# Performance work log

Hardware: AMD Instinct MI355X
Metric: run time of the kernel (lower is better)

The kernel has to match this reference:

```python
import jax, jax.numpy as jnp
import numpy as np

HEADS = 8
WS = 8  # window size


def conv1x1(x, w, b):
    # x: [B,C,H,W], w: [Cout,Cin], b: [Cout]
    return jnp.einsum('bchw,oc->bohw', x, w) + b[None, :, None, None]


def to_windows(x, heads, ws):
    # x: [B,C,H,W] -> [B*nH*nW, heads, ws*ws, C//heads]
    B, C, H, W = x.shape
    d = C // heads
    x = x.reshape(B, heads, d, H // ws, ws, W // ws, ws)
    x = x.transpose(0, 3, 5, 1, 4, 6, 2)  # B, nH, nW, heads, ws, ws, d
    return x.reshape(B * (H // ws) * (W // ws), heads, ws * ws, d)


def from_windows(xw, B, C, H, W, heads, ws):
    d = C // heads
    x = xw.reshape(B, H // ws, W // ws, heads, ws, ws, d)
    x = x.transpose(0, 3, 6, 1, 4, 2, 5)  # B, heads, d, nH, ws, nW, ws
    return x.reshape(B, C, H, W)


def setup_inputs() -> dict:
    key = jax.random.key(0)
    ks = jax.random.split(key, 10)
    B, C, H, W = 4, 256, 256, 256
    s = 0.02
    return {
        'q_feat': jax.random.normal(ks[0], (B, C, H, W), jnp.float32),
        'kv_feat': jax.random.normal(ks[1], (B, C, H, W), jnp.float32),
        'wq': jax.random.normal(ks[2], (C, C), jnp.float32) * s,
        'bq': jnp.zeros((C,), jnp.float32),
        'wk': jax.random.normal(ks[3], (C, C), jnp.float32) * s,
        'bk': jnp.zeros((C,), jnp.float32),
        'wv': jax.random.normal(ks[4], (C, C), jnp.float32) * s,
        'bv': jnp.zeros((C,), jnp.float32),
        'wp': jax.random.normal(ks[5], (C, C), jnp.float32) * s,
        'bp': jnp.zeros((C,), jnp.float32),
    }


def reference(q_feat, kv_feat, wq, bq, wk, bk, wv, bv, wp, bp):
    B, C, H, W = q_feat.shape
    heads, ws = HEADS, WS
    scale = (C // heads) ** (-0.5)

    q = to_windows(conv1x1(q_feat, wq, bq), heads, ws)   # [Nw, h, ws*ws, d]
    k = to_windows(conv1x1(kv_feat, wk, bk), heads, ws)
    v = to_windows(conv1x1(kv_feat, wv, bv), heads, ws)

    attn = jnp.einsum('whqd,whkd->whqk', q, k) * scale
    attn = jax.nn.softmax(attn, axis=-1)
    out_w = jnp.einsum('whqk,whkd->whqd', attn, v)

    out = from_windows(out_w, B, C, H, W, heads, ws)
    return conv1x1(out, wp, bp)
```

## Files before the change

kernel.cpp:

```cpp
#include <hip/hip_runtime.h>
#include <cstdint>
#include <cstddef>


typedef __attribute__((ext_vector_type(8))) short bfx8;
typedef __attribute__((ext_vector_type(4))) float f32x4;

#define HW 65536
#define NC 256
#define QKV_STRIDE 16777216UL

__device__ __forceinline__ unsigned short f2bf(float f) {
  union { float f; unsigned u; } v; v.f = f;
  unsigned r = v.u + 0x7FFFu + ((v.u >> 16) & 1u);
  return (unsigned short)(r >> 16);
}

__global__ __launch_bounds__(256) void prep_weights(
    const float* __restrict__ wq, const float* __restrict__ wk,
    const float* __restrict__ wv, const float* __restrict__ wp,
    unsigned short* __restrict__ dst) {
  int i = blockIdx.x * 256 + threadIdx.x;
  dst[i]          = f2bf(wq[i]);
  dst[i + 65536]  = f2bf(wk[i]);
  dst[i + 131072] = f2bf(wv[i]);
  dst[i + 196608] = f2bf(wp[i]);
}

__device__ __forceinline__ void gemm_pass(
    const unsigned short* __restrict__ wmat, const unsigned char* __restrict__ smem,
    int wid, int g, int qh, f32x4 (&acc)[4][4]) {
#pragma unroll
  for (int i = 0; i < 4; ++i)
#pragma unroll
    for (int j = 0; j < 4; ++j) acc[i][j] = (f32x4){0.f, 0.f, 0.f, 0.f};

  bfx8 afr[4];
#pragma unroll
  for (int mt = 0; mt < 4; ++mt)
    afr[mt] = *(const bfx8*)(wmat + (wid * 64 + mt * 16 + qh) * 256 + g * 8);

  for (int ks = 0; ks < 8; ++ks) {
    bfx8 naf[4];
    if (ks < 7) {
#pragma unroll
      for (int mt = 0; mt < 4; ++mt)
        naf[mt] = *(const bfx8*)(wmat + (wid * 64 + mt * 16 + qh) * 256 + (ks + 1) * 32 + g * 8);
    }
#pragma unroll
    for (int nt = 0; nt < 4; ++nt) {
      unsigned byte = ((unsigned)((nt * 16 + qh) * 512 + ks * 64 + g * 16)) ^
                      (((unsigned)(qh & 7)) << 4);
      bfx8 bfr = *(const bfx8*)(smem + byte);
#pragma unroll
      for (int mt = 0; mt < 4; ++mt)
        acc[mt][nt] = __builtin_amdgcn_mfma_f32_16x16x32_bf16(afr[mt], bfr, acc[mt][nt], 0, 0, 0);
    }
    if (ks < 7) {
#pragma unroll
      for (int mt = 0; mt < 4; ++mt) afr[mt] = naf[mt];
    }
  }
}

__device__ __forceinline__ void store_qk(
    const f32x4 (&acc)[4][4], const float* __restrict__ bias,
    unsigned short* __restrict__ outw, int n0, int wid, int g, int qh) {
  const int h_img = n0 >> 8, w0b = n0 & 255;
#pragma unroll
  for (int mt = 0; mt < 4; ++mt) {
    int o = wid * 64 + mt * 16 + g * 4;
    f32x4 bb = *(const f32x4*)&bias[o];
    int head = o >> 5, dbase = o & 31;
#pragma unroll
    for (int nt = 0; nt < 4; ++nt) {
      int n = nt * 16 + qh;
      int w_img = w0b + n;
      int win = ((h_img >> 3) << 5) + (w_img >> 3);
      int pos = ((h_img & 7) << 3) + (w_img & 7);
      f32x4 a = acc[mt][nt];
      uint2 pv;
      pv.x = (unsigned)f2bf(a.x + bb.x) | ((unsigned)f2bf(a.y + bb.y) << 16);
      pv.y = (unsigned)f2bf(a.z + bb.z) | ((unsigned)f2bf(a.w + bb.w) << 16);
      *(uint2*)&outw[((size_t)(win * 8 + head) * 64 + pos) * 32 + dbase] = pv;
    }
  }
}

__global__ __launch_bounds__(256) void qkv_gemm(
    const float* __restrict__ xq, const float* __restrict__ xkv,
    const unsigned short* __restrict__ wbf,
    const float* __restrict__ bq, const float* __restrict__ bk,
    const float* __restrict__ bv,
    unsigned short* __restrict__ q_w, unsigned short* __restrict__ k_w,
    unsigned short* __restrict__ v_w, int batch0, int batched) {
  __shared__ __align__(16) unsigned char smem[36864];

  const int tid = threadIdx.x;
  const int lane = tid & 63;
  const int wid = tid >> 6;
  const int g = lane >> 4;
  const int qh = lane & 15;
  const int mode = blockIdx.x & 1;
  const int n0 = (int)(blockIdx.x >> 1) * 64;
  const int batch = batch0 + blockIdx.z;
  const size_t qofs = batched ? (size_t)blockIdx.z * QKV_STRIDE : 0;
  const float* x = (mode ? xkv : xq) + (size_t)batch * NC * HW;

  {
    const int sn = tid & 63;
    const int oc = tid >> 6;
#pragma unroll
    for (int it = 0; it < 8; ++it) {
      int c8 = (it * 4 + oc) * 8;
      const float* xp = x + (size_t)c8 * HW + n0 + sn;
      float v0 = xp[0],      v1 = xp[HW],     v2 = xp[2 * HW], v3 = xp[3 * HW];
      float v4 = xp[4 * HW], v5 = xp[5 * HW], v6 = xp[6 * HW], v7 = xp[7 * HW];
      uint4 u;
      u.x = (unsigned)f2bf(v0) | ((unsigned)f2bf(v1) << 16);
      u.y = (unsigned)f2bf(v2) | ((unsigned)f2bf(v3) << 16);
      u.z = (unsigned)f2bf(v4) | ((unsigned)f2bf(v5) << 16);
      u.w = (unsigned)f2bf(v6) | ((unsigned)f2bf(v7) << 16);
      unsigned byte = ((unsigned)(sn * 512 + c8 * 2)) ^ (((unsigned)(sn & 7)) << 4);
      *(uint4*)(smem + byte) = u;
    }
  }
  __syncthreads();

  f32x4 acc[4][4];
  if (mode == 0) {
    gemm_pass(wbf, smem, wid, g, qh, acc);
    store_qk(acc, bq, q_w + qofs, n0, wid, g, qh);
  } else {
    gemm_pass(wbf + 65536, smem, wid, g, qh, acc);
    store_qk(acc, bk, k_w + qofs, n0, wid, g, qh);
    gemm_pass(wbf + 131072, smem, wid, g, qh, acc);
    __syncthreads();
    unsigned short* Vt = (unsigned short*)smem;
#pragma unroll
    for (int mt = 0; mt < 4; ++mt) {
      int o = wid * 64 + mt * 16 + g * 4;
      f32x4 bb = *(const f32x4*)&bv[o];
#pragma unroll
      for (int nt = 0; nt < 4; ++nt) {
        int n = nt * 16 + qh;
        f32x4 a = acc[mt][nt];
        Vt[(o + 0) * 72 + n] = f2bf(a.x + bb.x);
        Vt[(o + 1) * 72 + n] = f2bf(a.y + bb.y);
        Vt[(o + 2) * 72 + n] = f2bf(a.z + bb.z);
        Vt[(o + 3) * 72 + n] = f2bf(a.w + bb.w);
      }
    }
    __syncthreads();
    const int h_img = n0 >> 8, w0b = n0 & 255;
    unsigned short* vw = v_w + qofs;
#pragma unroll
    for (int it = 0; it < 8; ++it) {
      int id = it * 256 + tid;
      int o = id >> 3, oct = id & 7;
      uint4 val = *(const uint4*)&Vt[o * 72 + oct * 8];
      int head = o >> 5, dd = o & 31;
      int win = ((h_img >> 3) << 5) + (w0b >> 3) + oct;
      *(uint4*)&vw[((size_t)(win * 8 + head) * 32 + dd) * 64 + ((h_img & 7) << 3)] = val;
    }
  }
}

__global__ __launch_bounds__(256) void attn_conv(
    const unsigned short* __restrict__ q_w, const unsigned short* __restrict__ k_w,
    const unsigned short* __restrict__ v_w, const unsigned short* __restrict__ wpbf,
    const float* __restrict__ bp, float* __restrict__ out, int batch0, int batched) {
  __shared__ unsigned short P_lds[4][2048];
  __shared__ unsigned short y_t[16384];

  const int tid = threadIdx.x;
  const int lane = tid & 63;
  const int wid = tid >> 6;
  const int g = lane >> 4;
  const int qh = lane & 15;
  const int bid = blockIdx.x;
  const int winl = ((bid & 7) << 7) | (bid >> 3);
  const int batch = batch0 + blockIdx.z;
  const size_t qofs = batched ? (size_t)blockIdx.z * QKV_STRIDE : 0;
  const float scale = 0.17677669529663687f;

  char* pbase = (char*)&P_lds[wid][0];

#pragma unroll
  for (int hi = 0; hi < 2; ++hi) {
    const int head = wid + hi * 4;
    const unsigned short* qb = q_w + qofs + (size_t)(winl * 8 + head) * 2048;
    const unsigned short* kb = k_w + qofs + (size_t)(winl * 8 + head) * 2048;
    const unsigned short* vb = v_w + qofs + (size_t)(winl * 8 + head) * 2048;

    bfx8 kf[4], qf[4];
#pragma unroll
    for (int t = 0; t < 4; ++t) {
      kf[t] = *(const bfx8*)(kb + (t * 16 + qh) * 32 + g * 8);
      qf[t] = *(const bfx8*)(qb + (t * 16 + qh) * 32 + g * 8);
    }
    f32x4 zero = {0.f, 0.f, 0.f, 0.f};
    f32x4 st[4][4];
#pragma unroll
    for (int kt = 0; kt < 4; ++kt)
#pragma unroll
      for (int qt = 0; qt < 4; ++qt)
        st[kt][qt] = __builtin_amdgcn_mfma_f32_16x16x32_bf16(kf[kt], qf[qt], zero, 0, 0, 0);

    float rv[4];
#pragma unroll
    for (int qt = 0; qt < 4; ++qt) {
      float m = -1e30f;
#pragma unroll
      for (int kt = 0; kt < 4; ++kt) {
        f32x4 v = st[kt][qt];
        m = fmaxf(m, fmaxf(fmaxf(v.x, v.y), fmaxf(v.z, v.w)));
      }
      m = fmaxf(m, __shfl_xor(m, 16, 64));
      m = fmaxf(m, __shfl_xor(m, 32, 64));
      float ssum = 0.f;
#pragma unroll
      for (int kt = 0; kt < 4; ++kt) {
        f32x4 v = st[kt][qt], e;
        e.x = __expf((v.x - m) * scale);
        e.y = __expf((v.y - m) * scale);
        e.z = __expf((v.z - m) * scale);
        e.w = __expf((v.w - m) * scale);
        ssum += e.x + e.y + e.z + e.w;
        st[kt][qt] = e;
      }
      ssum += __shfl_xor(ssum, 16, 64);
      ssum += __shfl_xor(ssum, 32, 64);
      rv[qt] = 1.f / ssum;
    }

    f32x4 ot[2][4];
#pragma unroll
    for (int dt = 0; dt < 2; ++dt)
#pragma unroll
      for (int qt = 0; qt < 4; ++qt) ot[dt][qt] = zero;

#pragma unroll
    for (int s = 0; s < 2; ++s) {
#pragma unroll
      for (int qt = 0; qt < 4; ++qt) {
        int q = qt * 16 + qh;
        unsigned sw = ((unsigned)(q & 3)) << 4;
        float r = rv[qt];
#pragma unroll
        for (int k2 = 0; k2 < 2; ++k2) {
          f32x4 e = st[s * 2 + k2][qt];
          uint2 pv;
          pv.x = (unsigned)f2bf(e.x * r) | ((unsigned)f2bf(e.y * r) << 16);
          pv.y = (unsigned)f2bf(e.z * r) | ((unsigned)f2bf(e.w * r) << 16);
          unsigned byte = ((unsigned)q * 64 + (unsigned)(k2 * 32 + g * 8)) ^ sw;
          *(uint2*)(pbase + byte) = pv;
        }
      }
      bfx8 pf[4];
#pragma unroll
      for (int qt = 0; qt < 4; ++qt) {
        int q = qt * 16 + qh;
        unsigned byte = ((unsigned)q * 64 + (unsigned)(g * 16)) ^ (((unsigned)(q & 3)) << 4);
        pf[qt] = *(const bfx8*)(pbase + byte);
      }
#pragma unroll
      for (int dt = 0; dt < 2; ++dt) {
        bfx8 vf = *(const bfx8*)(vb + (dt * 16 + qh) * 64 + s * 32 + g * 8);
#pragma unroll
        for (int qt = 0; qt < 4; ++qt)
          ot[dt][qt] = __builtin_amdgcn_mfma_f32_16x16x32_bf16(vf, pf[qt], ot[dt][qt], 0, 0, 0);
      }
    }

#pragma unroll
    for (int dt = 0; dt < 2; ++dt) {
      int cb = head * 32 + dt * 16 + g * 4;
#pragma unroll
      for (int qt = 0; qt < 4; ++qt) {
        int pos = qt * 16 + qh;
        f32x4 a = ot[dt][qt];
        uint2 pv;
        pv.x = (unsigned)f2bf(a.x) | ((unsigned)f2bf(a.y) << 16);
        pv.y = (unsigned)f2bf(a.z) | ((unsigned)f2bf(a.w) << 16);
        unsigned byte = ((unsigned)pos * 512 + (unsigned)cb * 2) ^ (((unsigned)(pos & 7)) << 4);
        *(uint2*)((char*)y_t + byte) = pv;
      }
    }
  }
  __syncthreads();

  f32x4 acc[4][4];
#pragma unroll
  for (int i = 0; i < 4; ++i)
#pragma unroll
    for (int j = 0; j < 4; ++j) acc[i][j] = (f32x4){0.f, 0.f, 0.f, 0.f};

  for (int ks = 0; ks < 8; ++ks) {
    bfx8 af[4];
#pragma unroll
    for (int mt = 0; mt < 4; ++mt)
      af[mt] = *(const bfx8*)(wpbf + (wid * 64 + mt * 16 + qh) * 256 + ks * 32 + g * 8);
#pragma unroll
    for (int nt = 0; nt < 4; ++nt) {
      int pos = nt * 16 + qh;
      unsigned byte = ((unsigned)pos * 512 + (unsigned)(ks * 64 + g * 16)) ^ (((unsigned)(pos & 7)) << 4);
      bfx8 bfr = *(const bfx8*)((char*)y_t + byte);
#pragma unroll
      for (int mt = 0; mt < 4; ++mt)
        acc[mt][nt] = __builtin_amdgcn_mfma_f32_16x16x32_bf16(af[mt], bfr, acc[mt][nt], 0, 0, 0);
    }
  }

  const int wrow = winl >> 5, wcol = winl & 31;
  float* ob_ = out + (size_t)batch * NC * HW;
#pragma unroll
  for (int mt = 0; mt < 4; ++mt) {
    int o0 = wid * 64 + mt * 16 + g * 4;
    float b0 = bp[o0], b1 = bp[o0 + 1], b2 = bp[o0 + 2], b3 = bp[o0 + 3];
#pragma unroll
    for (int nt = 0; nt < 4; ++nt) {
      int pos = nt * 16 + qh;
      int h_img = wrow * 8 + (pos >> 3);
      int w_img = wcol * 8 + (pos & 7);
      float* pp = ob_ + (size_t)o0 * HW + h_img * 256 + w_img;
      pp[0]      = acc[mt][nt].x + b0;
      pp[HW]     = acc[mt][nt].y + b1;
      pp[2 * HW] = acc[mt][nt].z + b2;
      pp[3 * HW] = acc[mt][nt].w + b3;
    }
  }
}

extern "C" void kernel_launch(void* const* d_in, const int* in_sizes, int n_in,
                              void* d_out, int out_size, void* d_ws, size_t ws_size,
                              hipStream_t stream) {
  const float* q_feat = (const float*)d_in[0];
  const float* kv_feat = (const float*)d_in[1];
  const float* wq = (const float*)d_in[2];
  const float* bq = (const float*)d_in[3];
  const float* wk = (const float*)d_in[4];
  const float* bk = (const float*)d_in[5];
  const float* wv = (const float*)d_in[6];
  const float* bv = (const float*)d_in[7];
  const float* wp = (const float*)d_in[8];
  const float* bp = (const float*)d_in[9];
  float* out = (float*)d_out;

  unsigned short* wbf = (unsigned short*)d_ws;
  const size_t need_batched = 524288ul + 12ul * QKV_STRIDE * 2ul;

  hipLaunchKernelGGL(prep_weights, dim3(256), dim3(256), 0, stream, wq, wk, wv, wp, wbf);

  if (ws_size >= need_batched) {
    unsigned short* q_w = wbf + 262144;
    unsigned short* k_w = q_w + 4 * QKV_STRIDE;
    unsigned short* v_w = k_w + 4 * QKV_STRIDE;
    hipLaunchKernelGGL(qkv_gemm, dim3(2048, 1, 4), dim3(256), 0, stream,
                       q_feat, kv_feat, wbf, bq, bk, bv, q_w, k_w, v_w, 0, 1);
    hipLaunchKernelGGL(attn_conv, dim3(1024, 1, 4), dim3(256), 0, stream,
                       q_w, k_w, v_w, wbf + 196608, bp, out, 0, 1);
  } else {
    unsigned short* q_w = wbf + 262144;
    unsigned short* k_w = q_w + QKV_STRIDE;
    unsigned short* v_w = k_w + QKV_STRIDE;
    for (int b = 0; b < 4; ++b) {
      hipLaunchKernelGGL(qkv_gemm, dim3(2048, 1, 1), dim3(256), 0, stream,
                         q_feat, kv_feat, wbf, bq, bk, bv, q_w, k_w, v_w, b, 0);
      hipLaunchKernelGGL(attn_conv, dim3(1024, 1, 1), dim3(256), 0, stream,
                         q_w, k_w, v_w, wbf + 196608, bp, out, b, 0);
    }
  }
}
```

Baseline: 632.2 us.

## Pre-tile weights into MFMA fragment order and vectorize QKV input staging

The weight conversion kernel now writes bf16 weights in a per-lane MFMA fragment order, so each wave's A-operand loads become contiguous 16-byte-per-lane reads instead of strided row accesses. The QKV projection kernel now loads inputs as float4 along the spatial dimension, with each thread covering 16 channels. It uses a new LDS XOR swizzle (n ^ n>>2) to keep the transposed stores conflict-free. This aims to cut global load transactions and LDS bank conflicts, at the cost of more registers per thread for the staged inputs.

Result: slower. 645.2 us (+2.1%).

```diff
diff --git a/kernel.cpp b/kernel.cpp
--- a/kernel.cpp
+++ b/kernel.cpp
@@ -14,6 +14,10 @@
   union { float f; unsigned u; } v; v.f = f;
   unsigned r = v.u + 0x7FFFu + ((v.u >> 16) & 1u);
   return (unsigned short)(r >> 16);
+}
+
+__device__ __forceinline__ unsigned xswz(unsigned n) {
+  return ((n ^ (n >> 2)) & 7u) << 4;
 }
 
 __global__ __launch_bounds__(256) void prep_weights(
@@ -21,15 +25,17 @@
     const float* __restrict__ wv, const float* __restrict__ wp,
     unsigned short* __restrict__ dst) {
   int i = blockIdx.x * 256 + threadIdx.x;
-  dst[i]          = f2bf(wq[i]);
-  dst[i + 65536]  = f2bf(wk[i]);
-  dst[i + 131072] = f2bf(wv[i]);
-  dst[i + 196608] = f2bf(wp[i]);
+  int e = i & 7, lane = (i >> 3) & 63, ks = (i >> 9) & 7, ot = i >> 12;
+  int src = (ot * 16 + (lane & 15)) * 256 + ks * 32 + (lane >> 4) * 8 + e;
+  dst[i]          = f2bf(wq[src]);
+  dst[i + 65536]  = f2bf(wk[src]);
+  dst[i + 131072] = f2bf(wv[src]);
+  dst[i + 196608] = f2bf(wp[src]);
 }
 
 __device__ __forceinline__ void gemm_pass(
-    const unsigned short* __restrict__ wmat, const unsigned char* __restrict__ smem,
-    int wid, int g, int qh, f32x4 (&acc)[4][4]) {
+    const unsigned short* __restrict__ wT, const unsigned char* __restrict__ smem,
+    int wid, int lane, int g, int qh, f32x4 (&acc)[4][4]) {
 #pragma unroll
   for (int i = 0; i < 4; ++i)
 #pragma unroll
@@ -38,19 +44,19 @@
   bfx8 afr[4];
 #pragma unroll
   for (int mt = 0; mt < 4; ++mt)
-    afr[mt] = *(const bfx8*)(wmat + (wid * 64 + mt * 16 + qh) * 256 + g * 8);
+    afr[mt] = *(const bfx8*)(wT + (((wid * 4 + mt) * 8 + 0) * 64 + lane) * 8);
 
   for (int ks = 0; ks < 8; ++ks) {
     bfx8 naf[4];
     if (ks < 7) {
 #pragma unroll
       for (int mt = 0; mt < 4; ++mt)
-        naf[mt] = *(const bfx8*)(wmat + (wid * 64 + mt * 16 + qh) * 256 + (ks + 1) * 32 + g * 8);
+        naf[mt] = *(const bfx8*)(wT + (((wid * 4 + mt) * 8 + ks + 1) * 64 + lane) * 8);
     }
 #pragma unroll
     for (int nt = 0; nt < 4; ++nt) {
-      unsigned byte = ((unsigned)((nt * 16 + qh) * 512 + ks * 64 + g * 16)) ^
-                      (((unsigned)(qh & 7)) << 4);
+      unsigned n = (unsigned)(nt * 16 + qh);
+      unsigned byte = (n * 512 + (unsigned)(ks * 64 + g * 16)) ^ xswz(n);
       bfx8 bfr = *(const bfx8*)(smem + byte);
 #pragma unroll
       for (int mt = 0; mt < 4; ++mt)
@@ -108,33 +114,42 @@
   const float* x = (mode ? xkv : xq) + (size_t)batch * NC * HW;
 
   {
-    const int sn = tid & 63;
-    const int oc = tid >> 6;
-#pragma unroll
-    for (int it = 0; it < 8; ++it) {
-      int c8 = (it * 4 + oc) * 8;
-      const float* xp = x + (size_t)c8 * HW + n0 + sn;
-      float v0 = xp[0],      v1 = xp[HW],     v2 = xp[2 * HW], v3 = xp[3 * HW];
-      float v4 = xp[4 * HW], v5 = xp[5 * HW], v6 = xp[6 * HW], v7 = xp[7 * HW];
+    const int n4 = lane & 15;
+    const int c8a = wid * 4 + (lane >> 4);
+    const float* xp0 = x + (size_t)(c8a * 8) * HW + n0 + n4 * 4;
+    const float* xp1 = xp0 + (size_t)128 * HW;
+    f32x4 r0[8], r1[8];
+#pragma unroll
+    for (int i = 0; i < 8; ++i) r0[i] = *(const f32x4*)(xp0 + (size_t)i * HW);
+#pragma unroll
+    for (int i = 0; i < 8; ++i) r1[i] = *(const f32x4*)(xp1 + (size_t)i * HW);
+#pragma unroll
+    for (int e = 0; e < 4; ++e) {
+      unsigned n = (unsigned)(n4 * 4 + e);
       uint4 u;
-      u.x = (unsigned)f2bf(v0) | ((unsigned)f2bf(v1) << 16);
-      u.y = (unsigned)f2bf(v2) | ((unsigned)f2bf(v3) << 16);
-      u.z = (unsigned)f2bf(v4) | ((unsigned)f2bf(v5) << 16);
-      u.w = (unsigned)f2bf(v6) | ((unsigned)f2bf(v7) << 16);
-      unsigned byte = ((unsigned)(sn * 512 + c8 * 2)) ^ (((unsigned)(sn & 7)) << 4);
-      *(uint4*)(smem + byte) = u;
+      u.x = (unsigned)f2bf(r0[0][e]) | ((unsigned)f2bf(r0[1][e]) << 16);
+      u.y = (unsigned)f2bf(r0[2][e]) | ((unsigned)f2bf(r0[3][e]) << 16);
+      u.z = (unsigned)f2bf(r0[4][e]) | ((unsigned)f2bf(r0[5][e]) << 16);
+      u.w = (unsigned)f2bf(r0[6][e]) | ((unsigned)f2bf(r0[7][e]) << 16);
+      *(uint4*)(smem + ((n * 512 + (unsigned)c8a * 16) ^ xswz(n))) = u;
+      uint4 v;
+      v.x = (unsigned)f2bf(r1[0][e]) | ((unsigned)f2bf(r1[1][e]) << 16);
+      v.y = (unsigned)f2bf(r1[2][e]) | ((unsigned)f2bf(r1[3][e]) << 16);
+      v.z = (unsigned)f2bf(r1[4][e]) | ((unsigned)f2bf(r1[5][e]) << 16);
+      v.w = (unsigned)f2bf(r1[6][e]) | ((unsigned)f2bf(r1[7][e]) << 16);
+      *(uint4*)(smem + ((n * 512 + (unsigned)(c8a + 16) * 16) ^ xswz(n))) = v;
     }
   }
   __syncthreads();
 
   f32x4 acc[4][4];
   if (mode == 0) {
-    gemm_pass(wbf, smem, wid, g, qh, acc);
+    gemm_pass(wbf, smem, wid, lane, g, qh, acc);
     store_qk(acc, bq, q_w + qofs, n0, wid, g, qh);
   } else {
-    gemm_pass(wbf + 65536, smem, wid, g, qh, acc);
+    gemm_pass(wbf + 65536, smem, wid, lane, g, qh, acc);
     store_qk(acc, bk, k_w + qofs, n0, wid, g, qh);
-    gemm_pass(wbf + 131072, smem, wid, g, qh, acc);
+    gemm_pass(wbf + 131072, smem, wid, lane, g, qh, acc);
     __syncthreads();
     unsigned short* Vt = (unsigned short*)smem;
 #pragma unroll
@@ -168,7 +183,7 @@
 
 __global__ __launch_bounds__(256) void attn_conv(
     const unsigned short* __restrict__ q_w, const unsigned short* __restrict__ k_w,
-    const unsigned short* __restrict__ v_w, const unsigned short* __restrict__ wpbf,
+    const unsigned short* __restrict__ v_w, const unsigned short* __restrict__ wpT,
     const float* __restrict__ bp, float* __restrict__ out, int batch0, int batched) {
   __shared__ unsigned short P_lds[4][2048];
   __shared__ unsigned short y_t[16384];
@@ -300,7 +315,7 @@
     bfx8 af[4];
 #pragma unroll
     for (int mt = 0; mt < 4; ++mt)
-      af[mt] = *(const bfx8*)(wpbf + (wid * 64 + mt * 16 + qh) * 256 + ks * 32 + g * 8);
+      af[mt] = *(const bfx8*)(wpT + (((wid * 4 + mt) * 8 + ks) * 64 + lane) * 8);
 #pragma unroll
     for (int nt = 0; nt < 4; ++nt) {
       int pos = nt * 16 + qh;
```

## Stage Q/K stores through LDS, pre-swizzle Wp, process four windows per attention block

Applied to the files above, without the earlier changes.

The Q/K epilogue now writes its tiles into a separate LDS buffer and then emits 16-byte coalesced global stores per window/head row, replacing scattered 8-byte stores. The projection weight is pre-permuted into the MFMA fragment order so each lane loads its A fragment contiguously. The attention kernel now loops over four adjacent windows per block with a quarter of the blocks, which gives wider contiguous runs on output rows and reuses weight loads in cache. The cost is more LDS per block in qkv_gemm, which may lower occupancy, and fewer, longer attention blocks with extra barriers.

New measurement: 743.9 us. +17.7%, slower.

```diff
diff --git a/kernel.cpp b/kernel.cpp
--- a/kernel.cpp
+++ b/kernel.cpp
@@ -24,7 +24,29 @@
   dst[i]          = f2bf(wq[i]);
   dst[i + 65536]  = f2bf(wk[i]);
   dst[i + 131072] = f2bf(wv[i]);
-  dst[i + 196608] = f2bf(wp[i]);
+  int e = i & 7, lane = (i >> 3) & 63, ks = (i >> 9) & 7, ot = i >> 12;
+  int src = (ot * 16 + (lane & 15)) * 256 + ks * 32 + (lane >> 4) * 8 + e;
+  dst[i + 196608] = f2bf(wp[src]);
+}
+
+__device__ __forceinline__ void stage_x(
+    const float* __restrict__ x, int n0, int tid, unsigned char* __restrict__ smem) {
+  const int sn = tid & 63;
+  const int oc = tid >> 6;
+#pragma unroll
+  for (int it = 0; it < 8; ++it) {
+    int c8 = (it * 4 + oc) * 8;
+    const float* xp = x + (size_t)c8 * HW + n0 + sn;
+    float v0 = xp[0],      v1 = xp[HW],     v2 = xp[2 * HW], v3 = xp[3 * HW];
+    float v4 = xp[4 * HW], v5 = xp[5 * HW], v6 = xp[6 * HW], v7 = xp[7 * HW];
+    uint4 u;
+    u.x = (unsigned)f2bf(v0) | ((unsigned)f2bf(v1) << 16);
+    u.y = (unsigned)f2bf(v2) | ((unsigned)f2bf(v3) << 16);
+    u.z = (unsigned)f2bf(v4) | ((unsigned)f2bf(v5) << 16);
+    u.w = (unsigned)f2bf(v6) | ((unsigned)f2bf(v7) << 16);
+    unsigned byte = ((unsigned)(sn * 512 + c8 * 2)) ^ (((unsigned)(sn & 7)) << 4);
+    *(uint4*)(smem + byte) = u;
+  }
 }
 
 __device__ __forceinline__ void gemm_pass(
@@ -63,27 +85,41 @@
   }
 }
 
-__device__ __forceinline__ void store_qk(
+__device__ __forceinline__ void epi_qk_store(
     const f32x4 (&acc)[4][4], const float* __restrict__ bias,
-    unsigned short* __restrict__ outw, int n0, int wid, int g, int qh) {
-  const int h_img = n0 >> 8, w0b = n0 & 255;
+    unsigned short* __restrict__ outw, int n0, int wid, int g, int qh, int tid,
+    unsigned char* __restrict__ epi) {
+  const int h7 = (n0 >> 8) & 7;
+  const int w0b = n0 & 255;
 #pragma unroll
   for (int mt = 0; mt < 4; ++mt) {
     int o = wid * 64 + mt * 16 + g * 4;
     f32x4 bb = *(const f32x4*)&bias[o];
     int head = o >> 5, dbase = o & 31;
+    unsigned hs = (unsigned)(head & 7) << 4;
 #pragma unroll
     for (int nt = 0; nt < 4; ++nt) {
       int n = nt * 16 + qh;
-      int w_img = w0b + n;
-      int win = ((h_img >> 3) << 5) + (w_img >> 3);
-      int pos = ((h_img & 7) << 3) + (w_img & 7);
+      unsigned byte = ((unsigned)((n >> 3) * 4096 + head * 512 + (n & 7) * 64 + dbase * 2)) ^ hs;
       f32x4 a = acc[mt][nt];
       uint2 pv;
       pv.x = (unsigned)f2bf(a.x + bb.x) | ((unsigned)f2bf(a.y + bb.y) << 16);
       pv.y = (unsigned)f2bf(a.z + bb.z) | ((unsigned)f2bf(a.w + bb.w) << 16);
-      *(uint2*)&outw[((size_t)(win * 8 + head) * 64 + pos) * 32 + dbase] = pv;
-    }
+      *(uint2*)(epi + byte) = pv;
+    }
+  }
+  __syncthreads();
+  const int r = tid >> 2, lane4 = tid & 3;
+  const int winIdx = r >> 3, head = r & 7;
+  const unsigned hs = (unsigned)(head & 7) << 4;
+  const int win = ((n0 >> 8) >> 3) * 32 + (w0b >> 3) + winIdx;
+  unsigned short* gdst = outw + (size_t)(win * 8 + head) * 2048 + h7 * 256;
+  const unsigned char* src = epi + winIdx * 4096 + head * 512;
+#pragma unroll
+  for (int it = 0; it < 8; ++it) {
+    unsigned off = (unsigned)(it * 64 + lane4 * 16);
+    uint4 v = *(const uint4*)(src + (off ^ hs));
+    *(uint4*)&gdst[it * 32 + lane4 * 8] = v;
   }
 }
 
@@ -94,7 +130,8 @@
     const float* __restrict__ bv,
     unsigned short* __restrict__ q_w, unsigned short* __restrict__ k_w,
     unsigned short* __restrict__ v_w, int batch0, int batched) {
-  __shared__ __align__(16) unsigned char smem[36864];
+  __shared__ __align__(16) unsigned char smem[32768];
+  __shared__ __align__(16) unsigned char epi[36864];
 
   const int tid = threadIdx.x;
   const int lane = tid & 63;
@@ -107,36 +144,19 @@
   const size_t qofs = batched ? (size_t)blockIdx.z * QKV_STRIDE : 0;
   const float* x = (mode ? xkv : xq) + (size_t)batch * NC * HW;
 
-  {
-    const int sn = tid & 63;
-    const int oc = tid >> 6;
-#pragma unroll
-    for (int it = 0; it < 8; ++it) {
-      int c8 = (it * 4 + oc) * 8;
-      const float* xp = x + (size_t)c8 * HW + n0 + sn;
-      float v0 = xp[0],      v1 = xp[HW],     v2 = xp[2 * HW], v3 = xp[3 * HW];
-      float v4 = xp[4 * HW], v5 = xp[5 * HW], v6 = xp[6 * HW], v7 = xp[7 * HW];
-      uint4 u;
-      u.x = (unsigned)f2bf(v0) | ((unsigned)f2bf(v1) << 16);
-      u.y = (unsigned)f2bf(v2) | ((unsigned)f2bf(v3) << 16);
-      u.z = (unsigned)f2bf(v4) | ((unsigned)f2bf(v5) << 16);
-      u.w = (unsigned)f2bf(v6) | ((unsigned)f2bf(v7) << 16);
-      unsigned byte = ((unsigned)(sn * 512 + c8 * 2)) ^ (((unsigned)(sn & 7)) << 4);
-      *(uint4*)(smem + byte) = u;
-    }
-  }
+  stage_x(x, n0, tid, smem);
   __syncthreads();
 
   f32x4 acc[4][4];
   if (mode == 0) {
     gemm_pass(wbf, smem, wid, g, qh, acc);
-    store_qk(acc, bq, q_w + qofs, n0, wid, g, qh);
+    epi_qk_store(acc, bq, q_w + qofs, n0, wid, g, qh, tid, epi);
   } else {
     gemm_pass(wbf + 65536, smem, wid, g, qh, acc);
-    store_qk(acc, bk, k_w + qofs, n0, wid, g, qh);
+    epi_qk_store(acc, bk, k_w + qofs, n0, wid, g, qh, tid, epi);
     gemm_pass(wbf + 131072, smem, wid, g, qh, acc);
     __syncthreads();
-    unsigned short* Vt = (unsigned short*)smem;
+    unsigned short* Vt = (unsigned short*)epi;
 #pragma unroll
     for (int mt = 0; mt < 4; ++mt) {
       int o = wid * 64 + mt * 16 + g * 4;
@@ -168,7 +188,7 @@
 
 __global__ __launch_bounds__(256) void attn_conv(
     const unsigned short* __restrict__ q_w, const unsigned short* __restrict__ k_w,
-    const unsigned short* __restrict__ v_w, const unsigned short* __restrict__ wpbf,
+    const unsigned short* __restrict__ v_w, const unsigned short* __restrict__ wpT,
     const float* __restrict__ bp, float* __restrict__ out, int batch0, int batched) {
   __shared__ unsigned short P_lds[4][2048];
   __shared__ unsigned short y_t[16384];
@@ -179,155 +199,161 @@
   const int g = lane >> 4;
   const int qh = lane & 15;
   const int bid = blockIdx.x;
-  const int winl = ((bid & 7) << 7) | (bid >> 3);
+  const int wrow = bid >> 3;
+  const int wcol0 = (bid & 7) * 4;
   const int batch = batch0 + blockIdx.z;
   const size_t qofs = batched ? (size_t)blockIdx.z * QKV_STRIDE : 0;
   const float scale = 0.17677669529663687f;
 
   char* pbase = (char*)&P_lds[wid][0];
-
-#pragma unroll
-  for (int hi = 0; hi < 2; ++hi) {
-    const int head = wid + hi * 4;
-    const unsigned short* qb = q_w + qofs + (size_t)(winl * 8 + head) * 2048;
-    const unsigned short* kb = k_w + qofs + (size_t)(winl * 8 + head) * 2048;
-    const unsigned short* vb = v_w + qofs + (size_t)(winl * 8 + head) * 2048;
-
-    bfx8 kf[4], qf[4];
-#pragma unroll
-    for (int t = 0; t < 4; ++t) {
-      kf[t] = *(const bfx8*)(kb + (t * 16 + qh) * 32 + g * 8);
-      qf[t] = *(const bfx8*)(qb + (t * 16 + qh) * 32 + g * 8);
-    }
-    f32x4 zero = {0.f, 0.f, 0.f, 0.f};
-    f32x4 st[4][4];
-#pragma unroll
-    for (int kt = 0; kt < 4; ++kt)
-#pragma unroll
-      for (int qt = 0; qt < 4; ++qt)
-        st[kt][qt] = __builtin_amdgcn_mfma_f32_16x16x32_bf16(kf[kt], qf[qt], zero, 0, 0, 0);
-
-    float rv[4];
-#pragma unroll
-    for (int qt = 0; qt < 4; ++qt) {
-      float m = -1e30f;
-#pragma unroll
-      for (int kt = 0; kt < 4; ++kt) {
-        f32x4 v = st[kt][qt];
-        m = fmaxf(m, fmaxf(fmaxf(v.x, v.y), fmaxf(v.z, v.w)));
-      }
-      m = fmaxf(m, __shfl_xor(m, 16, 64));
-      m = fmaxf(m, __shfl_xor(m, 32, 64));
-      float ssum = 0.f;
-#pragma unroll
-      for (int kt = 0; kt < 4; ++kt) {
-        f32x4 v = st[kt][qt], e;
-        e.x = __expf((v.x - m) * scale);
-        e.y = __expf((v.y - m) * scale);
-        e.z = __expf((v.z - m) * scale);
-        e.w = __expf((v.w - m) * scale);
-        ssum += e.x + e.y + e.z + e.w;
-        st[kt][qt] = e;
-      }
-      ssum += __shfl_xor(ssum, 16, 64);
-      ssum += __shfl_xor(ssum, 32, 64);
-      rv[qt] = 1.f / ssum;
-    }
-
-    f32x4 ot[2][4];
-#pragma unroll
-    for (int dt = 0; dt < 2; ++dt)
-#pragma unroll
-      for (int qt = 0; qt < 4; ++qt) ot[dt][qt] = zero;
-
-#pragma unroll
-    for (int s = 0; s < 2; ++s) {
+  float* ob_ = out + (size_t)batch * NC * HW;
+
+  for (int wi = 0; wi < 4; ++wi) {
+    if (wi) __syncthreads();
+    const int winl = wrow * 32 + wcol0 + wi;
+
+#pragma unroll
+    for (int hi = 0; hi < 2; ++hi) {
+      const int head = wid + hi * 4;
+      const unsigned short* qb = q_w + qofs + (size_t)(winl * 8 + head) * 2048;
+      const unsigned short* kb = k_w + qofs + (size_t)(winl * 8 + head) * 2048;
+      const unsigned short* vb = v_w + qofs + (size_t)(winl * 8 + head) * 2048;
+
+      bfx8 kf[4], qf[4];
+#pragma unroll
+      for (int t = 0; t < 4; ++t) {
+        kf[t] = *(const bfx8*)(kb + (t * 16 + qh) * 32 + g * 8);
+        qf[t] = *(const bfx8*)(qb + (t * 16 + qh) * 32 + g * 8);
+      }
+      f32x4 zero = {0.f, 0.f, 0.f, 0.f};
+      f32x4 st[4][4];
+#pragma unroll
+      for (int kt = 0; kt < 4; ++kt)
+#pragma unroll
+        for (int qt = 0; qt < 4; ++qt)
+          st[kt][qt] = __builtin_amdgcn_mfma_f32_16x16x32_bf16(kf[kt], qf[qt], zero, 0, 0, 0);
+
+      float rv[4];
 #pragma unroll
       for (int qt = 0; qt < 4; ++qt) {
-        int q = qt * 16 + qh;
-        unsigned sw = ((unsigned)(q & 3)) << 4;
-        float r = rv[qt];
-#pragma unroll
-        for (int k2 = 0; k2 < 2; ++k2) {
-          f32x4 e = st[s * 2 + k2][qt];
+        float m = -1e30f;
+#pragma unroll
+        for (int kt = 0; kt < 4; ++kt) {
+          f32x4 v = st[kt][qt];
+          m = fmaxf(m, fmaxf(fmaxf(v.x, v.y), fmaxf(v.z, v.w)));
+        }
+        m = fmaxf(m, __shfl_xor(m, 16, 64));
+        m = fmaxf(m, __shfl_xor(m, 32, 64));
+        float ssum = 0.f;
+#pragma unroll
+        for (int kt = 0; kt < 4; ++kt) {
+          f32x4 v = st[kt][qt], e;
+          e.x = __expf((v.x - m) * scale);
+          e.y = __expf((v.y - m) * scale);
+          e.z = __expf((v.z - m) * scale);
+          e.w = __expf((v.w - m) * scale);
+          ssum += e.x + e.y + e.z + e.w;
+          st[kt][qt] = e;
+        }
+        ssum += __shfl_xor(ssum, 16, 64);
+        ssum += __shfl_xor(ssum, 32, 64);
+        rv[qt] = 1.f / ssum;
+      }
+
+      f32x4 ot[2][4];
+#pragma unroll
+      for (int dt = 0; dt < 2; ++dt)
+#pragma unroll
+        for (int qt = 0; qt < 4; ++qt) ot[dt][qt] = zero;
+
+#pragma unroll
+      for (int s = 0; s < 2; ++s) {
+#pragma unroll
+        for (int qt = 0; qt < 4; ++qt) {
+          int q = qt * 16 + qh;
+          unsigned sw = ((unsigned)(q & 3)) << 4;
+          float r = rv[qt];
+#pragma unroll
+          for (int k2 = 0; k2 < 2; ++k2) {
+            f32x4 e = st[s * 2 + k2][qt];
+            uint2 pv;
+            pv.x = (unsigned)f2bf(e.x * r) | ((unsigned)f2bf(e.y * r) << 16);
+            pv.y = (unsigned)f2bf(e.z * r) | ((unsigned)f2bf(e.w * r) << 16);
+            unsigned byte = ((unsigned)q * 64 + (unsigned)(k2 * 32 + g * 8)) ^ sw;
+            *(uint2*)(pbase + byte) = pv;
+          }
+        }
+        bfx8 pf[4];
+#pragma unroll
+        for (int qt = 0; qt < 4; ++qt) {
+          int q = qt * 16 + qh;
+          unsigned byte = ((unsigned)q * 64 + (unsigned)(g * 16)) ^ (((unsigned)(q & 3)) << 4);
+          pf[qt] = *(const bfx8*)(pbase + byte);
+        }
+#pragma unroll
+        for (int dt = 0; dt < 2; ++dt) {
+          bfx8 vf = *(const bfx8*)(vb + (dt * 16 + qh) * 64 + s * 32 + g * 8);
+#pragma unroll
+          for (int qt = 0; qt < 4; ++qt)
+            ot[dt][qt] = __builtin_amdgcn_mfma_f32_16x16x32_bf16(vf, pf[qt], ot[dt][qt], 0, 0, 0);
+        }
+      }
+
+#pragma unroll
+      for (int dt = 0; dt < 2; ++dt) {
+        int cb = head * 32 + dt * 16 + g * 4;
+#pragma unroll
+        for (int qt = 0; qt < 4; ++qt) {
+          int pos = qt * 16 + qh;
+          f32x4 a = ot[dt][qt];
           uint2 pv;
-          pv.x = (unsigned)f2bf(e.x * r) | ((unsigned)f2bf(e.y * r) << 16);
-          pv.y = (unsigned)f2bf(e.z * r) | ((unsigned)f2bf(e.w * r) << 16);
-          unsigned byte = ((unsigned)q * 64 + (unsigned)(k2 * 32 + g * 8)) ^ sw;
-          *(uint2*)(pbase + byte) = pv;
-        }
-      }
-      bfx8 pf[4];
-#pragma unroll
-      for (int qt = 0; qt < 4; ++qt) {
-        int q = qt * 16 + qh;
-        unsigned byte = ((unsigned)q * 64 + (unsigned)(g * 16)) ^ (((unsigned)(q & 3)) << 4);
-        pf[qt] = *(const bfx8*)(pbase + byte);
-      }
-#pragma unroll
-      for (int dt = 0; dt < 2; ++dt) {
-        bfx8 vf = *(const bfx8*)(vb + (dt * 16 + qh) * 64 + s * 32 + g * 8);
-#pragma unroll
-        for (int qt = 0; qt < 4; ++qt)
-          ot[dt][qt] = __builtin_amdgcn_mfma_f32_16x16x32_bf16(vf, pf[qt], ot[dt][qt], 0, 0, 0);
-      }
-    }
-
-#pragma unroll
-    for (int dt = 0; dt < 2; ++dt) {
-      int cb = head * 32 + dt * 16 + g * 4;
-#pragma unroll
-      for (int qt = 0; qt < 4; ++qt) {
-        int pos = qt * 16 + qh;
-        f32x4 a = ot[dt][qt];
-        uint2 pv;
-        pv.x = (unsigned)f2bf(a.x) | ((unsigned)f2bf(a.y) << 16);
-        pv.y = (unsigned)f2bf(a.z) | ((unsigned)f2bf(a.w) << 16);
-        unsigned byte = ((unsigned)pos * 512 + (unsigned)cb * 2) ^ (((unsigned)(pos & 7)) << 4);
-        *(uint2*)((char*)y_t + byte) = pv;
-      }
-    }
-  }
-  __syncthreads();
-
-  f32x4 acc[4][4];
-#pragma unroll
-  for (int i = 0; i < 4; ++i)
-#pragma unroll
-    for (int j = 0; j < 4; ++j) acc[i][j] = (f32x4){0.f, 0.f, 0.f, 0.f};
-
-  for (int ks = 0; ks < 8; ++ks) {
-    bfx8 af[4];
-#pragma unroll
-    for (int mt = 0; mt < 4; ++mt)
-      af[mt] = *(const bfx8*)(wpbf + (wid * 64 + mt * 16 + qh) * 256 + ks * 32 + g * 8);
-#pragma unroll
-    for (int nt = 0; nt < 4; ++nt) {
-      int pos = nt * 16 + qh;
-      unsigned byte = ((unsigned)pos * 512 + (unsigned)(ks * 64 + g * 16)) ^ (((unsigned)(pos & 7)) << 4);
-      bfx8 bfr = *(const bfx8*)((char*)y_t + byte);
+          pv.x = (unsigned)f2bf(a.x) | ((unsigned)f2bf(a.y) << 16);
+          pv.y = (unsigned)f2bf(a.z) | ((unsigned)f2bf(a.w) << 16);
+          unsigned byte = ((unsigned)pos * 512 + (unsigned)cb * 2) ^ (((unsigned)(pos & 7)) << 4);
+          *(uint2*)((char*)y_t + byte) = pv;
+        }
+      }
+    }
+    __syncthreads();
+
+    f32x4 acc[4][4];
+#pragma unroll
+    for (int i = 0; i < 4; ++i)
+#pragma unroll
+      for (int j = 0; j < 4; ++j) acc[i][j] = (f32x4){0.f, 0.f, 0.f, 0.f};
+
+    for (int ks = 0; ks < 8; ++ks) {
+      bfx8 af[4];
 #pragma unroll
       for (int mt = 0; mt < 4; ++mt)
-        acc[mt][nt] = __builtin_amdgcn_mfma_f32_16x16x32_bf16(af[mt], bfr, acc[mt][nt], 0, 0, 0);
-    }
-  }
-
-  const int wrow = winl >> 5, wcol = winl & 31;
-  float* ob_ = out + (size_t)batch * NC * HW;
-#pragma unroll
-  for (int mt = 0; mt < 4; ++mt) {
-    int o0 = wid * 64 + mt * 16 + g * 4;
-    float b0 = bp[o0], b1 = bp[o0 + 1], b2 = bp[o0 + 2], b3 = bp[o0 + 3];
-#pragma unroll
-    for (int nt = 0; nt < 4; ++nt) {
-      int pos = nt * 16 + qh;
-      int h_img = wrow * 8 + (pos >> 3);
-      int w_img = wcol * 8 + (pos & 7);
-      float* pp = ob_ + (size_t)o0 * HW + h_img * 256 + w_img;
-      pp[0]      = acc[mt][nt].x + b0;
-      pp[HW]     = acc[mt][nt].y + b1;
-      pp[2 * HW] = acc[mt][nt].z + b2;
-      pp[3 * HW] = acc[mt][nt].w + b3;
+        af[mt] = *(const bfx8*)(wpT + (((wid * 4 + mt) * 8 + ks) * 64 + lane) * 8);
+#pragma unroll
+      for (int nt = 0; nt < 4; ++nt) {
+        int pos = nt * 16 + qh;
+        unsigned byte = ((unsigned)pos * 512 + (unsigned)(ks * 64 + g * 16)) ^ (((unsigned)(pos & 7)) << 4);
+        bfx8 bfr = *(const bfx8*)((char*)y_t + byte);
+#pragma unroll
+        for (int mt = 0; mt < 4; ++mt)
+          acc[mt][nt] = __builtin_amdgcn_mfma_f32_16x16x32_bf16(af[mt], bfr, acc[mt][nt], 0, 0, 0);
+      }
+    }
+
+    const int wcol = wcol0 + wi;
+#pragma unroll
+    for (int mt = 0; mt < 4; ++mt) {
+      int o0 = wid * 64 + mt * 16 + g * 4;
+      float b0 = bp[o0], b1 = bp[o0 + 1], b2 = bp[o0 + 2], b3 = bp[o0 + 3];
+#pragma unroll
+      for (int nt = 0; nt < 4; ++nt) {
+        int pos = nt * 16 + qh;
+        int h_img = wrow * 8 + (pos >> 3);
+        int w_img = wcol * 8 + (pos & 7);
+        float* pp = ob_ + (size_t)o0 * HW + h_img * 256 + w_img;
+        pp[0]      = acc[mt][nt].x + b0;
+        pp[HW]     = acc[mt][nt].y + b1;
+        pp[2 * HW] = acc[mt][nt].z + b2;
+        pp[3 * HW] = acc[mt][nt].w + b3;
+      }
     }
   }
 }
@@ -358,7 +384,7 @@
     unsigned short* v_w = k_w + 4 * QKV_STRIDE;
     hipLaunchKernelGGL(qkv_gemm, dim3(2048, 1, 4), dim3(256), 0, stream,
                        q_feat, kv_feat, wbf, bq, bk, bv, q_w, k_w, v_w, 0, 1);
-    hipLaunchKernelGGL(attn_conv, dim3(1024, 1, 4), dim3(256), 0, stream,
+    hipLaunchKernelGGL(attn_conv, dim3(256, 1, 4), dim3(256), 0, stream,
                        q_w, k_w, v_w, wbf + 196608, bp, out, 0, 1);
   } else {
     unsigned short* q_w = wbf + 262144;
@@ -367,7 +393,7 @@
     for (int b = 0; b < 4; ++b) {
       hipLaunchKernelGGL(qkv_gemm, dim3(2048, 1, 1), dim3(256), 0, stream,
                          q_feat, kv_feat, wbf, bq, bk, bv, q_w, k_w, v_w, b, 0);
-      hipLaunchKernelGGL(attn_conv, dim3(1024, 1, 1), dim3(256), 0, stream,
+      hipLaunchKernelGGL(attn_conv, dim3(256, 1, 1), dim3(256), 0, stream,
                          q_w, k_w, v_w, wbf + 196608, bp, out, b, 0);
     }
   }
```

## Merge Q and KV projection blocks and pre-swizzle Wp for fragment loads

Applied to the files above, without the earlier changes.

The qkv_gemm kernel now has each block stage both the q and kv input tiles into two 32KB LDS buffers and compute Q, K and V itself, instead of splitting Q and KV work across alternating blocks. This balances per-block work (previously KV blocks did twice the GEMMs of Q blocks) and halves the grid. The V transpose buffer now reuses bufQ with an XOR swizzle to reduce LDS bank conflicts. The projection weight Wp is also pre-permuted into MFMA fragment order so attn_conv loads it with contiguous per-lane reads. The trade-off is that 64KB of LDS per block lowers occupancy and gives fewer, longer blocks.

New measurement: 605.4 us. 4.2% less time.

```diff
diff --git a/kernel.cpp b/kernel.cpp
--- a/kernel.cpp
+++ b/kernel.cpp
@@ -24,7 +24,29 @@
   dst[i]          = f2bf(wq[i]);
   dst[i + 65536]  = f2bf(wk[i]);
   dst[i + 131072] = f2bf(wv[i]);
-  dst[i + 196608] = f2bf(wp[i]);
+  int e = i & 7, lane = (i >> 3) & 63, ks = (i >> 9) & 7, ot = i >> 12;
+  int src = (ot * 16 + (lane & 15)) * 256 + ks * 32 + (lane >> 4) * 8 + e;
+  dst[i + 196608] = f2bf(wp[src]);
+}
+
+__device__ __forceinline__ void stage_x(
+    const float* __restrict__ x, int n0, int tid, unsigned char* __restrict__ smem) {
+  const int sn = tid & 63;
+  const int oc = tid >> 6;
+#pragma unroll
+  for (int it = 0; it < 8; ++it) {
+    int c8 = (it * 4 + oc) * 8;
+    const float* xp = x + (size_t)c8 * HW + n0 + sn;
+    float v0 = xp[0],      v1 = xp[HW],     v2 = xp[2 * HW], v3 = xp[3 * HW];
+    float v4 = xp[4 * HW], v5 = xp[5 * HW], v6 = xp[6 * HW], v7 = xp[7 * HW];
+    uint4 u;
+    u.x = (unsigned)f2bf(v0) | ((unsigned)f2bf(v1) << 16);
+    u.y = (unsigned)f2bf(v2) | ((unsigned)f2bf(v3) << 16);
+    u.z = (unsigned)f2bf(v4) | ((unsigned)f2bf(v5) << 16);
+    u.w = (unsigned)f2bf(v6) | ((unsigned)f2bf(v7) << 16);
+    unsigned byte = ((unsigned)(sn * 512 + c8 * 2)) ^ (((unsigned)(sn & 7)) << 4);
+    *(uint4*)(smem + byte) = u;
+  }
 }
 
 __device__ __forceinline__ void gemm_pass(
@@ -94,81 +116,68 @@
     const float* __restrict__ bv,
     unsigned short* __restrict__ q_w, unsigned short* __restrict__ k_w,
     unsigned short* __restrict__ v_w, int batch0, int batched) {
-  __shared__ __align__(16) unsigned char smem[36864];
+  __shared__ __align__(16) unsigned char bufQ[32768];
+  __shared__ __align__(16) unsigned char bufKV[32768];
 
   const int tid = threadIdx.x;
   const int lane = tid & 63;
   const int wid = tid >> 6;
   const int g = lane >> 4;
   const int qh = lane & 15;
-  const int mode = blockIdx.x & 1;
-  const int n0 = (int)(blockIdx.x >> 1) * 64;
+  const int n0 = (int)blockIdx.x * 64;
   const int batch = batch0 + blockIdx.z;
   const size_t qofs = batched ? (size_t)blockIdx.z * QKV_STRIDE : 0;
-  const float* x = (mode ? xkv : xq) + (size_t)batch * NC * HW;
-
-  {
-    const int sn = tid & 63;
-    const int oc = tid >> 6;
-#pragma unroll
-    for (int it = 0; it < 8; ++it) {
-      int c8 = (it * 4 + oc) * 8;
-      const float* xp = x + (size_t)c8 * HW + n0 + sn;
-      float v0 = xp[0],      v1 = xp[HW],     v2 = xp[2 * HW], v3 = xp[3 * HW];
-      float v4 = xp[4 * HW], v5 = xp[5 * HW], v6 = xp[6 * HW], v7 = xp[7 * HW];
-      uint4 u;
-      u.x = (unsigned)f2bf(v0) | ((unsigned)f2bf(v1) << 16);
-      u.y = (unsigned)f2bf(v2) | ((unsigned)f2bf(v3) << 16);
-      u.z = (unsigned)f2bf(v4) | ((unsigned)f2bf(v5) << 16);
-      u.w = (unsigned)f2bf(v6) | ((unsigned)f2bf(v7) << 16);
-      unsigned byte = ((unsigned)(sn * 512 + c8 * 2)) ^ (((unsigned)(sn & 7)) << 4);
-      *(uint4*)(smem + byte) = u;
-    }
-  }
+  const float* xq_b = xq + (size_t)batch * NC * HW;
+  const float* xkv_b = xkv + (size_t)batch * NC * HW;
+
+  stage_x(xq_b, n0, tid, bufQ);
+  stage_x(xkv_b, n0, tid, bufKV);
   __syncthreads();
 
   f32x4 acc[4][4];
-  if (mode == 0) {
-    gemm_pass(wbf, smem, wid, g, qh, acc);
-    store_qk(acc, bq, q_w + qofs, n0, wid, g, qh);
-  } else {
-    gemm_pass(wbf + 65536, smem, wid, g, qh, acc);
-    store_qk(acc, bk, k_w + qofs, n0, wid, g, qh);
-    gemm_pass(wbf + 131072, smem, wid, g, qh, acc);
-    __syncthreads();
-    unsigned short* Vt = (unsigned short*)smem;
-#pragma unroll
-    for (int mt = 0; mt < 4; ++mt) {
-      int o = wid * 64 + mt * 16 + g * 4;
-      f32x4 bb = *(const f32x4*)&bv[o];
-#pragma unroll
-      for (int nt = 0; nt < 4; ++nt) {
-        int n = nt * 16 + qh;
-        f32x4 a = acc[mt][nt];
-        Vt[(o + 0) * 72 + n] = f2bf(a.x + bb.x);
-        Vt[(o + 1) * 72 + n] = f2bf(a.y + bb.y);
-        Vt[(o + 2) * 72 + n] = f2bf(a.z + bb.z);
-        Vt[(o + 3) * 72 + n] = f2bf(a.w + bb.w);
-      }
-    }
-    __syncthreads();
-    const int h_img = n0 >> 8, w0b = n0 & 255;
-    unsigned short* vw = v_w + qofs;
-#pragma unroll
-    for (int it = 0; it < 8; ++it) {
-      int id = it * 256 + tid;
-      int o = id >> 3, oct = id & 7;
-      uint4 val = *(const uint4*)&Vt[o * 72 + oct * 8];
-      int head = o >> 5, dd = o & 31;
-      int win = ((h_img >> 3) << 5) + (w0b >> 3) + oct;
-      *(uint4*)&vw[((size_t)(win * 8 + head) * 32 + dd) * 64 + ((h_img & 7) << 3)] = val;
-    }
+  gemm_pass(wbf, bufQ, wid, g, qh, acc);
+  store_qk(acc, bq, q_w + qofs, n0, wid, g, qh);
+  gemm_pass(wbf + 65536, bufKV, wid, g, qh, acc);
+  store_qk(acc, bk, k_w + qofs, n0, wid, g, qh);
+  gemm_pass(wbf + 131072, bufKV, wid, g, qh, acc);
+
+  __syncthreads();
+#pragma unroll
+  for (int mt = 0; mt < 4; ++mt) {
+    int o = wid * 64 + mt * 16 + g * 4;
+    f32x4 bb = *(const f32x4*)&bv[o];
+#pragma unroll
+    for (int nt = 0; nt < 4; ++nt) {
+      int n = nt * 16 + qh;
+      f32x4 a = acc[mt][nt];
+      float vj[4] = {a.x + bb.x, a.y + bb.y, a.z + bb.z, a.w + bb.w};
+#pragma unroll
+      for (int j = 0; j < 4; ++j) {
+        unsigned oo = (unsigned)(o + j);
+        unsigned byte = (oo * 128 + (unsigned)n * 2) ^ (((oo >> 2) & 7u) << 4);
+        *(unsigned short*)(bufQ + byte) = f2bf(vj[j]);
+      }
+    }
+  }
+  __syncthreads();
+  const int h_img = n0 >> 8, w0b = n0 & 255;
+  unsigned short* vw = v_w + qofs;
+#pragma unroll
+  for (int it = 0; it < 8; ++it) {
+    int id = it * 256 + tid;
+    unsigned o = (unsigned)(id >> 3);
+    int oct = id & 7;
+    unsigned byte = (o * 128 + (unsigned)oct * 16) ^ (((o >> 2) & 7u) << 4);
+    uint4 val = *(const uint4*)(bufQ + byte);
+    int head = (int)(o >> 5), dd = (int)(o & 31);
+    int win = ((h_img >> 3) << 5) + (w0b >> 3) + oct;
+    *(uint4*)&vw[((size_t)(win * 8 + head) * 32 + dd) * 64 + ((h_img & 7) << 3)] = val;
   }
 }
 
 __global__ __launch_bounds__(256) void attn_conv(
     const unsigned short* __restrict__ q_w, const unsigned short* __restrict__ k_w,
-    const unsigned short* __restrict__ v_w, const unsigned short* __restrict__ wpbf,
+    const unsigned short* __restrict__ v_w, const unsigned short* __restrict__ wpT,
     const float* __restrict__ bp, float* __restrict__ out, int batch0, int batched) {
   __shared__ unsigned short P_lds[4][2048];
   __shared__ unsigned short y_t[16384];
@@ -300,7 +309,7 @@
     bfx8 af[4];
 #pragma unroll
     for (int mt = 0; mt < 4; ++mt)
-      af[mt] = *(const bfx8*)(wpbf + (wid * 64 + mt * 16 + qh) * 256 + ks * 32 + g * 8);
+      af[mt] = *(const bfx8*)(wpT + (((wid * 4 + mt) * 8 + ks) * 64 + lane) * 8);
 #pragma unroll
     for (int nt = 0; nt < 4; ++nt) {
       int pos = nt * 16 + qh;
@@ -356,7 +365,7 @@
     unsigned short* q_w = wbf + 262144;
     unsigned short* k_w = q_w + 4 * QKV_STRIDE;
     unsigned short* v_w = k_w + 4 * QKV_STRIDE;
-    hipLaunchKernelGGL(qkv_gemm, dim3(2048, 1, 4), dim3(256), 0, stream,
+    hipLaunchKernelGGL(qkv_gemm, dim3(1024, 1, 4), dim3(256), 0, stream,
                        q_feat, kv_feat, wbf, bq, bk, bv, q_w, k_w, v_w, 0, 1);
     hipLaunchKernelGGL(attn_conv, dim3(1024, 1, 4), dim3(256), 0, stream,
                        q_w, k_w, v_w, wbf + 196608, bp, out, 0, 1);
@@ -365,7 +374,7 @@
     unsigned short* k_w = q_w + QKV_STRIDE;
     unsigned short* v_w = k_w + QKV_STRIDE;
     for (int b = 0; b < 4; ++b) {
-      hipLaunchKernelGGL(qkv_gemm, dim3(2048, 1, 1), dim3(256), 0, stream,
+      hipLaunchKernelGGL(qkv_gemm, dim3(1024, 1, 1), dim3(256), 0, stream,
                          q_feat, kv_feat, wbf, bq, bk, bv, q_w, k_w, v_w, b, 0);
       hipLaunchKernelGGL(attn_conv, dim3(1024, 1, 1), dim3(256), 0, stream,
                          q_w, k_w, v_w, wbf + 196608, bp, out, b, 0);
```
